# Optimization experiments

Hardware: AMD Instinct MI355X
Metric: run time of the kernel (lower is better)

The kernel has to match this reference:

```python
import jax, jax.numpy as jnp
import numpy as np


def setup_inputs() -> dict:
    key = jax.random.key(0)
    ks = jax.random.split(key, 8)
    C, CK = 512, 64  # channels, att_channels = channels // 8
    B, H, W = 8, 64, 64
    x = jax.random.normal(ks[0], (B, C, H, W), dtype=jnp.float32)
    # 1x1 conv weights stored as [out, in] matrices
    s_in = 1.0 / np.sqrt(C)
    Wf_w = jax.random.uniform(ks[1], (CK, C), jnp.float32, -s_in, s_in)
    Wf_b = jax.random.uniform(ks[2], (CK,), jnp.float32, -s_in, s_in)
    Wg_w = jax.random.uniform(ks[3], (CK, C), jnp.float32, -s_in, s_in)
    Wg_b = jax.random.uniform(ks[4], (CK,), jnp.float32, -s_in, s_in)
    Wh_w = jax.random.uniform(ks[5], (C, C), jnp.float32, -s_in, s_in)
    Wh_b = jax.random.uniform(ks[6], (C,), jnp.float32, -s_in, s_in)
    gamma = jax.random.normal(ks[7], (1,), dtype=jnp.float32) * 0.1
    return {"x": x, "Wf_w": Wf_w, "Wf_b": Wf_b, "Wg_w": Wg_w, "Wg_b": Wg_b,
            "Wh_w": Wh_w, "Wh_b": Wh_b, "gamma": gamma}


def reference(x, Wf_w, Wf_b, Wg_w, Wg_b, Wh_w, Wh_b, gamma):
    B, C, H, W = x.shape
    N = H * W
    xt = x.reshape(B, C, N).transpose(0, 2, 1)           # [B, N, C]
    f = xt @ Wf_w.T + Wf_b                                # [B, N, Ck]
    g = xt @ Wg_w.T + Wg_b                                # [B, N, Ck]
    h = xt @ Wh_w.T + Wh_b                                # [B, N, C]
    scores = jnp.einsum('bnk,bmk->bnm', f, g)             # f @ g^T -> [B, N, N]
    beta = jax.nn.softmax(scores, axis=2)
    o = jnp.einsum('bnm,bmc->bnc', beta, h)               # [B, N, C]
    o = o.transpose(0, 2, 1).reshape(B, C, H, W)
    return gamma[0] * o + x
```

## Files before the change

kernel.cpp:

```cpp
#include <hip/hip_runtime.h>

typedef __attribute__((ext_vector_type(8))) short bf16x8;
typedef __attribute__((ext_vector_type(4))) float f32x4;
typedef __attribute__((ext_vector_type(16))) float f32x16;
typedef unsigned short u16;
typedef unsigned int u32;

namespace {
constexpr int kB = 8;
constexpr int kC = 512;
constexpr int kCK = 64;
constexpr int kN = 4096;

__device__ __forceinline__ u16 f2bf(float f) {
  union { float f; u32 u; } v; v.f = f;
  u32 r = v.u + 0x7fffu + ((v.u >> 16) & 1u);
  return (u16)(r >> 16);
}
__device__ __forceinline__ u32 pk2bf(float a, float b) {
  return (u32)f2bf(a) | ((u32)f2bf(b) << 16);
}
__device__ __forceinline__ f32x4 zero4() { f32x4 z = {0.f, 0.f, 0.f, 0.f}; return z; }
}

__global__ __launch_bounds__(256)
void wcast_kernel(const float* __restrict__ Wf, const float* __restrict__ Wg,
                  const float* __restrict__ Wh, u16* __restrict__ Wcat)
{
  const int idx = blockIdx.x * 256 + threadIdx.x;
  const int e = idx * 4;
  const int row = e >> 9, col = e & 511;
  const float* src = (row < 64) ? &Wf[(size_t)row * 512 + col]
                   : (row < 128) ? &Wg[(size_t)(row - 64) * 512 + col]
                                 : &Wh[(size_t)(row - 128) * 512 + col];
  const float4 v = *(const float4*)src;
  uint2 pk;
  pk.x = pk2bf(v.x, v.y);
  pk.y = pk2bf(v.z, v.w);
  *(uint2*)&Wcat[e] = pk;
}

__global__ __launch_bounds__(256, 2)
void fused_proj_kernel(const float* __restrict__ x, const u16* __restrict__ Wcat,
                       const float* __restrict__ Wf_b, const float* __restrict__ Wg_b,
                       const float* __restrict__ Wh_b,
                       u16* __restrict__ F, u16* __restrict__ G, u16* __restrict__ HT)
{
  const int t = threadIdx.x;
  const int nt = blockIdx.x, b = blockIdx.y;
  const int wave = t >> 6, lane = t & 63, lq = lane & 15, lk = lane >> 4;

  __shared__ __align__(16) u16 xt[64][536];

  const float* xb = x + (size_t)b * kC * kN + (size_t)nt * 64;
  for (int c0 = 0; c0 < kC; c0 += 16) {
    const int c = c0 + wave * 4;
    const size_t base = (size_t)c * kN + lane;
    const float v0 = xb[base];
    const float v1 = xb[base + kN];
    const float v2 = xb[base + 2 * (size_t)kN];
    const float v3 = xb[base + 3 * (size_t)kN];
    uint2 pk; pk.x = pk2bf(v0, v1); pk.y = pk2bf(v2, v3);
    *(uint2*)&xt[lane][c] = pk;
  }
  __syncthreads();

  f32x4 accF[4], accG[4], accH[8][4];
#pragma unroll
  for (int ni = 0; ni < 4; ++ni) { accF[ni] = zero4(); accG[ni] = zero4(); }
#pragma unroll
  for (int cj = 0; cj < 8; ++cj)
#pragma unroll
    for (int ni = 0; ni < 4; ++ni) accH[cj][ni] = zero4();

  for (int ks = 0; ks < 16; ++ks) {
    const int kb = ks * 32 + lk * 8;
    bf16x8 xf[4];
#pragma unroll
    for (int ni = 0; ni < 4; ++ni)
      xf[ni] = *(const bf16x8*)&xt[ni * 16 + lq][kb];

    const bf16x8 wf = *(const bf16x8*)&Wcat[(size_t)(wave * 16 + lq) * 512 + kb];
    const bf16x8 wg = *(const bf16x8*)&Wcat[(size_t)(64 + wave * 16 + lq) * 512 + kb];
    bf16x8 wh[8];
#pragma unroll
    for (int cj = 0; cj < 8; ++cj)
      wh[cj] = *(const bf16x8*)&Wcat[(size_t)(128 + wave * 128 + cj * 16 + lq) * 512 + kb];

#pragma unroll
    for (int ni = 0; ni < 4; ++ni) {
      accF[ni] = __builtin_amdgcn_mfma_f32_16x16x32_bf16(wf, xf[ni], accF[ni], 0, 0, 0);
      accG[ni] = __builtin_amdgcn_mfma_f32_16x16x32_bf16(wg, xf[ni], accG[ni], 0, 0, 0);
#pragma unroll
      for (int cj = 0; cj < 8; ++cj)
        accH[cj][ni] = __builtin_amdgcn_mfma_f32_16x16x32_bf16(xf[ni], wh[cj], accH[cj][ni], 0, 0, 0);
    }
  }

  u16* Fb = F + (size_t)b * kN * kCK;
  u16* Gb = G + (size_t)b * kN * kCK;
  u16* Hb = HT + (size_t)b * kC * kN;

  {
    const float4 bf = *(const float4*)&Wf_b[wave * 16 + lk * 4];
    const float4 bg = *(const float4*)&Wg_b[wave * 16 + lk * 4];
#pragma unroll
    for (int ni = 0; ni < 4; ++ni) {
      const size_t nrow = (size_t)(nt * 64 + ni * 16 + lq);
      uint2 pf, pg;
      pf.x = pk2bf(accF[ni][0] + bf.x, accF[ni][1] + bf.y);
      pf.y = pk2bf(accF[ni][2] + bf.z, accF[ni][3] + bf.w);
      pg.x = pk2bf(accG[ni][0] + bg.x, accG[ni][1] + bg.y);
      pg.y = pk2bf(accG[ni][2] + bg.z, accG[ni][3] + bg.w);
      *(uint2*)&Fb[nrow * kCK + wave * 16 + lk * 4] = pf;
      *(uint2*)&Gb[nrow * kCK + wave * 16 + lk * 4] = pg;
    }
  }
#pragma unroll
  for (int cj = 0; cj < 8; ++cj) {
    const int cout = wave * 128 + cj * 16 + lq;
    const float bh = Wh_b[cout];
#pragma unroll
    for (int ni = 0; ni < 4; ++ni) {
      uint2 ph;
      ph.x = pk2bf(accH[cj][ni][0] + bh, accH[cj][ni][1] + bh);
      ph.y = pk2bf(accH[cj][ni][2] + bh, accH[cj][ni][3] + bh);
      *(uint2*)&Hb[(size_t)cout * kN + nt * 64 + ni * 16 + lk * 4] = ph;
    }
  }
}

__global__ __launch_bounds__(512, 2)
void pv_kernel(const float* __restrict__ x, const u16* __restrict__ F,
               const u16* __restrict__ G, const u16* __restrict__ HT,
               const float* __restrict__ gamma, float* __restrict__ out)
{
  const int t = threadIdx.x;
  const int bid = blockIdx.x;
  const int b  = bid & 7;
  const int qt = bid >> 3;
  const int wave = t >> 6, lane = t & 63;
  const int lq = lane & 15, lk = lane >> 4;
  const int l31 = lane & 31, hi = lane >> 5;

  const int sq2 = wave & 3;
  const int sm2 = wave >> 2;

  const u16* Fb = F + (size_t)b * kN * kCK;
  const u16* Gb = G + (size_t)b * kN * kCK;
  const u16* Hb = HT + (size_t)b * kC * kN;

  __shared__ __align__(16) u16 Ps[2][128][72];
  __shared__ float Lred[2][128];

  const float g0 = gamma[0];

  bf16x8 fF[2][2];
#pragma unroll
  for (int ct = 0; ct < 2; ++ct)
#pragma unroll
    for (int kh = 0; kh < 2; ++kh)
      fF[ct][kh] = *(const bf16x8*)&Fb[(size_t)(qt * 128 + sq2 * 32 + ct * 16 + lq) * kCK + lk * 8 + kh * 32];

  f32x16 acc[2][4];
#pragma unroll
  for (int ci = 0; ci < 2; ++ci)
#pragma unroll
    for (int qb = 0; qb < 4; ++qb)
#pragma unroll
      for (int r = 0; r < 16; ++r) acc[ci][qb][r] = 0.f;

  float lsum[2] = {0.f, 0.f};

  bf16x8 gc[2][2];
#pragma unroll
  for (int ms = 0; ms < 2; ++ms)
#pragma unroll
    for (int kh = 0; kh < 2; ++kh)
      gc[ms][kh] = *(const bf16x8*)&Gb[(size_t)(sm2 * 32 + ms * 16 + lq) * kCK + lk * 8 + kh * 32];

  bf16x8 hc[2][4];

  {
    f32x4 s[2][2];
#pragma unroll
    for (int ms = 0; ms < 2; ++ms)
#pragma unroll
      for (int ct = 0; ct < 2; ++ct) {
        s[ms][ct] = zero4();
        s[ms][ct] = __builtin_amdgcn_mfma_f32_16x16x32_bf16(gc[ms][0], fF[ct][0], s[ms][ct], 0, 0, 0);
        s[ms][ct] = __builtin_amdgcn_mfma_f32_16x16x32_bf16(gc[ms][1], fF[ct][1], s[ms][ct], 0, 0, 0);
      }
#pragma unroll
    for (int ms = 0; ms < 2; ++ms)
#pragma unroll
      for (int kh = 0; kh < 2; ++kh)
        gc[ms][kh] = *(const bf16x8*)&Gb[(size_t)(64 + sm2 * 32 + ms * 16 + lq) * kCK + lk * 8 + kh * 32];
#pragma unroll
    for (int ms = 0; ms < 2; ++ms)
#pragma unroll
      for (int ct = 0; ct < 2; ++ct) {
        const float p0 = __expf(s[ms][ct][0]);
        const float p1 = __expf(s[ms][ct][1]);
        const float p2 = __expf(s[ms][ct][2]);
        const float p3 = __expf(s[ms][ct][3]);
        lsum[ct] += (p0 + p1) + (p2 + p3);
        uint2 pk; pk.x = pk2bf(p0, p1); pk.y = pk2bf(p2, p3);
        *(uint2*)&Ps[0][sq2 * 32 + ct * 16 + lq][sm2 * 32 + ms * 16 + lk * 4] = pk;
      }
#pragma unroll
    for (int ci = 0; ci < 2; ++ci) {
      const size_t hrow = (size_t)(wave * 64 + ci * 32 + l31) * kN;
#pragma unroll
      for (int ks = 0; ks < 4; ++ks)
        hc[ci][ks] = *(const bf16x8*)&Hb[hrow + ks * 16 + hi * 8];
    }
    asm volatile("s_waitcnt lgkmcnt(0)\n\ts_barrier" ::: "memory");
  }

  for (int mt = 1; mt < kN / 64; ++mt) {
    const int pb = (mt - 1) & 1;
    const int buf = mt & 1;

    f32x4 s[2][2];
#pragma unroll
    for (int ms = 0; ms < 2; ++ms)
#pragma unroll
      for (int ct = 0; ct < 2; ++ct) {
        s[ms][ct] = zero4();
        s[ms][ct] = __builtin_amdgcn_mfma_f32_16x16x32_bf16(gc[ms][0], fF[ct][0], s[ms][ct], 0, 0, 0);
        s[ms][ct] = __builtin_amdgcn_mfma_f32_16x16x32_bf16(gc[ms][1], fF[ct][1], s[ms][ct], 0, 0, 0);
      }

    {
      const int mtn = (mt + 1 < kN / 64) ? mt + 1 : mt;
#pragma unroll
      for (int ms = 0; ms < 2; ++ms)
#pragma unroll
        for (int kh = 0; kh < 2; ++kh)
          gc[ms][kh] = *(const bf16x8*)&Gb[(size_t)(mtn * 64 + sm2 * 32 + ms * 16 + lq) * kCK + lk * 8 + kh * 32];
    }

#pragma unroll
    for (int ks = 0; ks < 4; ++ks) {
      bf16x8 pB[4];
#pragma unroll
      for (int qb = 0; qb < 4; ++qb)
        pB[qb] = *(const bf16x8*)&Ps[pb][qb * 32 + l31][ks * 16 + hi * 8];
      {
        const int ms = ks >> 1, ct = ks & 1;
        const float p0 = __expf(s[ms][ct][0]);
        const float p1 = __expf(s[ms][ct][1]);
        const float p2 = __expf(s[ms][ct][2]);
        const float p3 = __expf(s[ms][ct][3]);
        lsum[ct] += (p0 + p1) + (p2 + p3);
        uint2 pk; pk.x = pk2bf(p0, p1); pk.y = pk2bf(p2, p3);
        *(uint2*)&Ps[buf][sq2 * 32 + ct * 16 + lq][sm2 * 32 + ms * 16 + lk * 4] = pk;
      }
      __builtin_amdgcn_s_setprio(1);
#pragma unroll
      for (int ci = 0; ci < 2; ++ci)
#pragma unroll
        for (int qb = 0; qb < 4; ++qb)
          acc[ci][qb] = __builtin_amdgcn_mfma_f32_32x32x16_bf16(hc[ci][ks], pB[qb], acc[ci][qb], 0, 0, 0);
      __builtin_amdgcn_s_setprio(0);
    }

#pragma unroll
    for (int ci = 0; ci < 2; ++ci) {
      const size_t hrow = (size_t)(wave * 64 + ci * 32 + l31) * kN + (size_t)mt * 64;
#pragma unroll
      for (int ks = 0; ks < 4; ++ks)
        hc[ci][ks] = *(const bf16x8*)&Hb[hrow + ks * 16 + hi * 8];
    }

    asm volatile("s_waitcnt lgkmcnt(0)\n\ts_barrier" ::: "memory");
  }

  {
    const int pb = (kN / 64 - 1) & 1;
#pragma unroll
    for (int ks = 0; ks < 4; ++ks) {
      bf16x8 pB[4];
#pragma unroll
      for (int qb = 0; qb < 4; ++qb)
        pB[qb] = *(const bf16x8*)&Ps[pb][qb * 32 + l31][ks * 16 + hi * 8];
#pragma unroll
      for (int ci = 0; ci < 2; ++ci)
#pragma unroll
        for (int qb = 0; qb < 4; ++qb)
          acc[ci][qb] = __builtin_amdgcn_mfma_f32_32x32x16_bf16(hc[ci][ks], pB[qb], acc[ci][qb], 0, 0, 0);
    }
  }

  float l0 = lsum[0], l1 = lsum[1];
  l0 += __shfl_xor(l0, 16); l0 += __shfl_xor(l0, 32);
  l1 += __shfl_xor(l1, 16); l1 += __shfl_xor(l1, 32);
  __syncthreads();
  if (lane < 16) {
    Lred[sm2][sq2 * 32 + lane] = l0;
    Lred[sm2][sq2 * 32 + 16 + lane] = l1;
  }
  __syncthreads();

  float rs[4];
#pragma unroll
  for (int qb = 0; qb < 4; ++qb)
    rs[qb] = 1.f / (Lred[0][qb * 32 + l31] + Lred[1][qb * 32 + l31]);

#pragma unroll
  for (int ci = 0; ci < 2; ++ci)
#pragma unroll
    for (int qb = 0; qb < 4; ++qb)
#pragma unroll
      for (int r = 0; r < 16; ++r) {
        const int crow = (r & 3) + 8 * (r >> 2) + 4 * hi;
        const int c = wave * 64 + ci * 32 + crow;
        const int n = qt * 128 + qb * 32 + l31;
        const size_t idx = ((size_t)b * kC + c) * kN + n;
        out[idx] = g0 * (acc[ci][qb][r] * rs[qb]) + x[idx];
      }
}

extern "C" void kernel_launch(void* const* d_in, const int* in_sizes, int n_in,
                              void* d_out, int out_size, void* d_ws, size_t ws_size,
                              hipStream_t stream)
{
  const float* x     = (const float*)d_in[0];
  const float* Wf_w  = (const float*)d_in[1];
  const float* Wf_b  = (const float*)d_in[2];
  const float* Wg_w  = (const float*)d_in[3];
  const float* Wg_b  = (const float*)d_in[4];
  const float* Wh_w  = (const float*)d_in[5];
  const float* Wh_b  = (const float*)d_in[6];
  const float* gamma = (const float*)d_in[7];
  float* out = (float*)d_out;

  const size_t nF = (size_t)kB * kN * kCK;
  const size_t nH = (size_t)kB * kC * kN;
  const size_t nW = 640 * 512;

  u16* F  = (u16*)d_ws;
  u16* G  = F + nF;
  u16* HT = G + nF;
  u16* Wcat = HT + nH;
  const size_t need = (2 * nF + nH + nW) * sizeof(u16);
  if (ws_size < need) return;

  wcast_kernel<<<dim3(nW / 1024), dim3(256), 0, stream>>>(Wf_w, Wg_w, Wh_w, Wcat);
  fused_proj_kernel<<<dim3(kN / 64, kB), dim3(256), 0, stream>>>(x, Wcat, Wf_b, Wg_b, Wh_b, F, G, HT);
  pv_kernel<<<dim3(256), dim3(512), 0, stream>>>(x, F, G, HT, gamma, out);
}
```

Measured before the change: 254.2 us.

## Split pv_kernel into smaller query tiles and channel halves for more blocks

Shrinks the pv_kernel tile from 128 queries by all 512 channels to 64 queries by 256 channels, and launches 1024 blocks instead of 256. Accumulator registers drop, so launch bounds rise to 4 blocks per CU for higher occupancy and better fill of the 256 CUs. The cost is redundant work: each channel half recomputes the full F·G^T scores and exponentials, and G and H tiles are reloaded by more blocks, so compute per output and memory traffic both go up.

```diff
diff --git a/kernel.cpp b/kernel.cpp
--- a/kernel.cpp
+++ b/kernel.cpp
@@ -130,7 +130,7 @@
   }
 }
 
-__global__ __launch_bounds__(512, 2)
+__global__ __launch_bounds__(512, 4)
 void pv_kernel(const float* __restrict__ x, const u16* __restrict__ F,
                const u16* __restrict__ G, const u16* __restrict__ HT,
                const float* __restrict__ gamma, float* __restrict__ out)
@@ -138,7 +138,8 @@
   const int t = threadIdx.x;
   const int bid = blockIdx.x;
   const int b  = bid & 7;
-  const int qt = bid >> 3;
+  const int qt = (bid >> 3) & 63;
+  const int cs = bid >> 9;
   const int wave = t >> 6, lane = t & 63;
   const int lq = lane & 15, lk = lane >> 4;
   const int l31 = lane & 31, hi = lane >> 5;
@@ -150,27 +151,23 @@
   const u16* Gb = G + (size_t)b * kN * kCK;
   const u16* Hb = HT + (size_t)b * kC * kN;
 
-  __shared__ __align__(16) u16 Ps[2][128][72];
-  __shared__ float Lred[2][128];
+  __shared__ __align__(16) u16 Ps[2][64][72];
+  __shared__ float Lred[2][64];
 
   const float g0 = gamma[0];
 
-  bf16x8 fF[2][2];
-#pragma unroll
-  for (int ct = 0; ct < 2; ++ct)
-#pragma unroll
-    for (int kh = 0; kh < 2; ++kh)
-      fF[ct][kh] = *(const bf16x8*)&Fb[(size_t)(qt * 128 + sq2 * 32 + ct * 16 + lq) * kCK + lk * 8 + kh * 32];
-
-  f32x16 acc[2][4];
-#pragma unroll
-  for (int ci = 0; ci < 2; ++ci)
-#pragma unroll
-    for (int qb = 0; qb < 4; ++qb)
-#pragma unroll
-      for (int r = 0; r < 16; ++r) acc[ci][qb][r] = 0.f;
-
-  float lsum[2] = {0.f, 0.f};
+  bf16x8 fF[2];
+#pragma unroll
+  for (int kh = 0; kh < 2; ++kh)
+    fF[kh] = *(const bf16x8*)&Fb[(size_t)(qt * 64 + sq2 * 16 + lq) * kCK + lk * 8 + kh * 32];
+
+  f32x16 acc[2];
+#pragma unroll
+  for (int qb = 0; qb < 2; ++qb)
+#pragma unroll
+    for (int r = 0; r < 16; ++r) acc[qb][r] = 0.f;
+
+  float lsum = 0.f;
 
   bf16x8 gc[2][2];
 #pragma unroll
@@ -179,42 +176,35 @@
     for (int kh = 0; kh < 2; ++kh)
       gc[ms][kh] = *(const bf16x8*)&Gb[(size_t)(sm2 * 32 + ms * 16 + lq) * kCK + lk * 8 + kh * 32];
 
-  bf16x8 hc[2][4];
+  bf16x8 hc[4];
+  const size_t hrow_base = (size_t)(cs * 256 + wave * 32 + l31) * kN;
 
   {
-    f32x4 s[2][2];
-#pragma unroll
-    for (int ms = 0; ms < 2; ++ms)
-#pragma unroll
-      for (int ct = 0; ct < 2; ++ct) {
-        s[ms][ct] = zero4();
-        s[ms][ct] = __builtin_amdgcn_mfma_f32_16x16x32_bf16(gc[ms][0], fF[ct][0], s[ms][ct], 0, 0, 0);
-        s[ms][ct] = __builtin_amdgcn_mfma_f32_16x16x32_bf16(gc[ms][1], fF[ct][1], s[ms][ct], 0, 0, 0);
-      }
+    f32x4 s[2];
+#pragma unroll
+    for (int ms = 0; ms < 2; ++ms) {
+      s[ms] = zero4();
+      s[ms] = __builtin_amdgcn_mfma_f32_16x16x32_bf16(gc[ms][0], fF[0], s[ms], 0, 0, 0);
+      s[ms] = __builtin_amdgcn_mfma_f32_16x16x32_bf16(gc[ms][1], fF[1], s[ms], 0, 0, 0);
+    }
 #pragma unroll
     for (int ms = 0; ms < 2; ++ms)
 #pragma unroll
       for (int kh = 0; kh < 2; ++kh)
         gc[ms][kh] = *(const bf16x8*)&Gb[(size_t)(64 + sm2 * 32 + ms * 16 + lq) * kCK + lk * 8 + kh * 32];
 #pragma unroll
-    for (int ms = 0; ms < 2; ++ms)
-#pragma unroll
-      for (int ct = 0; ct < 2; ++ct) {
-        const float p0 = __expf(s[ms][ct][0]);
-        const float p1 = __expf(s[ms][ct][1]);
-        const float p2 = __expf(s[ms][ct][2]);
-        const float p3 = __expf(s[ms][ct][3]);
-        lsum[ct] += (p0 + p1) + (p2 + p3);
-        uint2 pk; pk.x = pk2bf(p0, p1); pk.y = pk2bf(p2, p3);
-        *(uint2*)&Ps[0][sq2 * 32 + ct * 16 + lq][sm2 * 32 + ms * 16 + lk * 4] = pk;
-      }
-#pragma unroll
-    for (int ci = 0; ci < 2; ++ci) {
-      const size_t hrow = (size_t)(wave * 64 + ci * 32 + l31) * kN;
-#pragma unroll
-      for (int ks = 0; ks < 4; ++ks)
-        hc[ci][ks] = *(const bf16x8*)&Hb[hrow + ks * 16 + hi * 8];
-    }
+    for (int ms = 0; ms < 2; ++ms) {
+      const float p0 = __expf(s[ms][0]);
+      const float p1 = __expf(s[ms][1]);
+      const float p2 = __expf(s[ms][2]);
+      const float p3 = __expf(s[ms][3]);
+      lsum += (p0 + p1) + (p2 + p3);
+      uint2 pk; pk.x = pk2bf(p0, p1); pk.y = pk2bf(p2, p3);
+      *(uint2*)&Ps[0][sq2 * 16 + lq][sm2 * 32 + ms * 16 + lk * 4] = pk;
+    }
+#pragma unroll
+    for (int ks = 0; ks < 4; ++ks)
+      hc[ks] = *(const bf16x8*)&Hb[hrow_base + ks * 16 + hi * 8];
     asm volatile("s_waitcnt lgkmcnt(0)\n\ts_barrier" ::: "memory");
   }
 
@@ -222,15 +212,13 @@
     const int pb = (mt - 1) & 1;
     const int buf = mt & 1;
 
-    f32x4 s[2][2];
-#pragma unroll
-    for (int ms = 0; ms < 2; ++ms)
-#pragma unroll
-      for (int ct = 0; ct < 2; ++ct) {
-        s[ms][ct] = zero4();
-        s[ms][ct] = __builtin_amdgcn_mfma_f32_16x16x32_bf16(gc[ms][0], fF[ct][0], s[ms][ct], 0, 0, 0);
-        s[ms][ct] = __builtin_amdgcn_mfma_f32_16x16x32_bf16(gc[ms][1], fF[ct][1], s[ms][ct], 0, 0, 0);
-      }
+    f32x4 s[2];
+#pragma unroll
+    for (int ms = 0; ms < 2; ++ms) {
+      s[ms] = zero4();
+      s[ms] = __builtin_amdgcn_mfma_f32_16x16x32_bf16(gc[ms][0], fF[0], s[ms], 0, 0, 0);
+      s[ms] = __builtin_amdgcn_mfma_f32_16x16x32_bf16(gc[ms][1], fF[1], s[ms], 0, 0, 0);
+    }
 
     {
       const int mtn = (mt + 1 < kN / 64) ? mt + 1 : mt;
@@ -243,36 +231,30 @@
 
 #pragma unroll
     for (int ks = 0; ks < 4; ++ks) {
-      bf16x8 pB[4];
-#pragma unroll
-      for (int qb = 0; qb < 4; ++qb)
+      bf16x8 pB[2];
+#pragma unroll
+      for (int qb = 0; qb < 2; ++qb)
         pB[qb] = *(const bf16x8*)&Ps[pb][qb * 32 + l31][ks * 16 + hi * 8];
-      {
-        const int ms = ks >> 1, ct = ks & 1;
-        const float p0 = __expf(s[ms][ct][0]);
-        const float p1 = __expf(s[ms][ct][1]);
-        const float p2 = __expf(s[ms][ct][2]);
-        const float p3 = __expf(s[ms][ct][3]);
-        lsum[ct] += (p0 + p1) + (p2 + p3);
+      if ((ks & 1) == 0) {
+        const int ms = ks >> 1;
+        const float p0 = __expf(s[ms][0]);
+        const float p1 = __expf(s[ms][1]);
+        const float p2 = __expf(s[ms][2]);
+        const float p3 = __expf(s[ms][3]);
+        lsum += (p0 + p1) + (p2 + p3);
         uint2 pk; pk.x = pk2bf(p0, p1); pk.y = pk2bf(p2, p3);
-        *(uint2*)&Ps[buf][sq2 * 32 + ct * 16 + lq][sm2 * 32 + ms * 16 + lk * 4] = pk;
+        *(uint2*)&Ps[buf][sq2 * 16 + lq][sm2 * 32 + ms * 16 + lk * 4] = pk;
       }
       __builtin_amdgcn_s_setprio(1);
 #pragma unroll
-      for (int ci = 0; ci < 2; ++ci)
-#pragma unroll
-        for (int qb = 0; qb < 4; ++qb)
-          acc[ci][qb] = __builtin_amdgcn_mfma_f32_32x32x16_bf16(hc[ci][ks], pB[qb], acc[ci][qb], 0, 0, 0);
+      for (int qb = 0; qb < 2; ++qb)
+        acc[qb] = __builtin_amdgcn_mfma_f32_32x32x16_bf16(hc[ks], pB[qb], acc[qb], 0, 0, 0);
       __builtin_amdgcn_s_setprio(0);
     }
 
 #pragma unroll
-    for (int ci = 0; ci < 2; ++ci) {
-      const size_t hrow = (size_t)(wave * 64 + ci * 32 + l31) * kN + (size_t)mt * 64;
-#pragma unroll
-      for (int ks = 0; ks < 4; ++ks)
-        hc[ci][ks] = *(const bf16x8*)&Hb[hrow + ks * 16 + hi * 8];
-    }
+    for (int ks = 0; ks < 4; ++ks)
+      hc[ks] = *(const bf16x8*)&Hb[hrow_base + (size_t)mt * 64 + ks * 16 + hi * 8];
 
     asm volatile("s_waitcnt lgkmcnt(0)\n\ts_barrier" ::: "memory");
   }
@@ -281,45 +263,37 @@
     const int pb = (kN / 64 - 1) & 1;
 #pragma unroll
     for (int ks = 0; ks < 4; ++ks) {
-      bf16x8 pB[4];
-#pragma unroll
-      for (int qb = 0; qb < 4; ++qb)
+      bf16x8 pB[2];
+#pragma unroll
+      for (int qb = 0; qb < 2; ++qb)
         pB[qb] = *(const bf16x8*)&Ps[pb][qb * 32 + l31][ks * 16 + hi * 8];
 #pragma unroll
-      for (int ci = 0; ci < 2; ++ci)
-#pragma unroll
-        for (int qb = 0; qb < 4; ++qb)
-          acc[ci][qb] = __builtin_amdgcn_mfma_f32_32x32x16_bf16(hc[ci][ks], pB[qb], acc[ci][qb], 0, 0, 0);
-    }
-  }
-
-  float l0 = lsum[0], l1 = lsum[1];
+      for (int qb = 0; qb < 2; ++qb)
+        acc[qb] = __builtin_amdgcn_mfma_f32_32x32x16_bf16(hc[ks], pB[qb], acc[qb], 0, 0, 0);
+    }
+  }
+
+  float l0 = lsum;
   l0 += __shfl_xor(l0, 16); l0 += __shfl_xor(l0, 32);
-  l1 += __shfl_xor(l1, 16); l1 += __shfl_xor(l1, 32);
   __syncthreads();
-  if (lane < 16) {
-    Lred[sm2][sq2 * 32 + lane] = l0;
-    Lred[sm2][sq2 * 32 + 16 + lane] = l1;
-  }
+  if (lane < 16) Lred[sm2][sq2 * 16 + lane] = l0;
   __syncthreads();
 
-  float rs[4];
-#pragma unroll
-  for (int qb = 0; qb < 4; ++qb)
+  float rs[2];
+#pragma unroll
+  for (int qb = 0; qb < 2; ++qb)
     rs[qb] = 1.f / (Lred[0][qb * 32 + l31] + Lred[1][qb * 32 + l31]);
 
 #pragma unroll
-  for (int ci = 0; ci < 2; ++ci)
-#pragma unroll
-    for (int qb = 0; qb < 4; ++qb)
-#pragma unroll
-      for (int r = 0; r < 16; ++r) {
-        const int crow = (r & 3) + 8 * (r >> 2) + 4 * hi;
-        const int c = wave * 64 + ci * 32 + crow;
-        const int n = qt * 128 + qb * 32 + l31;
-        const size_t idx = ((size_t)b * kC + c) * kN + n;
-        out[idx] = g0 * (acc[ci][qb][r] * rs[qb]) + x[idx];
-      }
+  for (int qb = 0; qb < 2; ++qb)
+#pragma unroll
+    for (int r = 0; r < 16; ++r) {
+      const int crow = (r & 3) + 8 * (r >> 2) + 4 * hi;
+      const int c = cs * 256 + wave * 32 + crow;
+      const int n = qt * 64 + qb * 32 + l31;
+      const size_t idx = ((size_t)b * kC + c) * kN + n;
+      out[idx] = g0 * (acc[qb][r] * rs[qb]) + x[idx];
+    }
 }
 
 extern "C" void kernel_launch(void* const* d_in, const int* in_sizes, int n_in,
@@ -349,5 +323,5 @@
 
   wcast_kernel<<<dim3(nW / 1024), dim3(256), 0, stream>>>(Wf_w, Wg_w, Wh_w, Wcat);
   fused_proj_kernel<<<dim3(kN / 64, kB), dim3(256), 0, stream>>>(x, Wcat, Wf_b, Wg_b, Wh_b, F, G, HT);
-  pv_kernel<<<dim3(256), dim3(512), 0, stream>>>(x, F, G, HT, gamma, out);
-}
+  pv_kernel<<<dim3(1024), dim3(512), 0, stream>>>(x, F, G, HT, gamma, out);
+}
```

After: 521.0 us. 105% more time.
